# Kernel optimization log

Hardware: AMD Instinct MI355X
Metric: run time of the kernel (lower is better)

## Reference

```python
import jax, jax.numpy as jnp
import numpy as np

B, T, C_EMBD, C_ATT = 16, 1024, 2048, 2048


def wkv(time_decay, time_first, k, v):
    """Numerically-stable RWKV WKV recurrence (matches wkv_cuda).
    time_decay/time_first: [C]; k, v: [B, T, C] -> y: [B, T, C]."""
    w = -jnp.exp(time_decay)  # [C], decay is -exp(param)
    u = time_first
    Bn, Tn, Cn = k.shape

    def step(carry, kv_t):
        aa, bb, pp = carry          # each [B, C]
        kt, vt = kv_t               # [B, C]
        ww = u + kt
        p = jnp.maximum(pp, ww)
        e1 = jnp.exp(pp - p)
        e2 = jnp.exp(ww - p)
        y = (e1 * aa + e2 * vt) / (e1 * bb + e2)
        ww2 = pp + w
        p2 = jnp.maximum(ww2, kt)
        e1b = jnp.exp(ww2 - p2)
        e2b = jnp.exp(kt - p2)
        new = (e1b * aa + e2b * vt, e1b * bb + e2b, p2)
        return new, y

    init = (jnp.zeros((Bn, Cn), k.dtype),
            jnp.zeros((Bn, Cn), k.dtype),
            jnp.full((Bn, Cn), -1e38, k.dtype))
    kT = jnp.swapaxes(k, 0, 1)  # [T, B, C]
    vT = jnp.swapaxes(v, 0, 1)
    _, ys = jax.lax.scan(step, init, (kT, vT))
    return jnp.swapaxes(ys, 0, 1)  # [B, T, C]


def setup_inputs() -> dict:
    key = jax.random.key(0)
    ks = jax.random.split(key, 10)
    xav = np.sqrt(2.0 / (C_EMBD + C_ATT))
    inp = {
        "x": jax.random.normal(ks[0], (B, T, C_EMBD), jnp.float32),
        "time_decay": jax.random.normal(ks[1], (C_ATT,), jnp.float32) * 0.02,
        "time_first": jax.random.normal(ks[2], (C_ATT,), jnp.float32) * 0.02,
        "time_mix_k": jax.random.normal(ks[3], (1, 1, C_EMBD), jnp.float32) * 0.02,
        "time_mix_v": jax.random.normal(ks[4], (1, 1, C_EMBD), jnp.float32) * 0.02,
        "time_mix_r": jax.random.normal(ks[5], (1, 1, C_EMBD), jnp.float32) * 0.02,
        "key_w": jax.random.normal(ks[6], (C_ATT, C_EMBD), jnp.float32) * xav,
        "value_w": jax.random.normal(ks[7], (C_ATT, C_EMBD), jnp.float32) * xav,
        "receptance_w": jax.random.normal(ks[8], (C_ATT, C_EMBD), jnp.float32) * xav,
        "output_w": jax.random.normal(ks[9], (C_EMBD, C_ATT), jnp.float32) * xav,
    }
    return inp


def reference(x, time_decay, time_first, time_mix_k, time_mix_v, time_mix_r,
              key_w, value_w, receptance_w, output_w):
    # time shift: xx[:, t] = x[:, t-1], xx[:, 0] = 0
    xx = jnp.pad(x, ((0, 0), (1, 0), (0, 0)))[:, :-1]
    xk = x * time_mix_k + xx * (1 - time_mix_k)
    xv = x * time_mix_v + xx * (1 - time_mix_v)
    xr = x * time_mix_r + xx * (1 - time_mix_r)
    k = jnp.einsum('btc,dc->btd', xk, key_w)
    v = jnp.einsum('btc,dc->btd', xv, value_w)
    r = jnp.einsum('btc,dc->btd', xr, receptance_w)
    sr = jax.nn.sigmoid(r)
    rwkv = sr * wkv(time_decay, time_first, k, v)
    return jnp.einsum('btd,cd->btc', rwkv, output_w)
```

## Files before the change

### kernel.cpp

```cpp
#include <hip/hip_runtime.h>
#include <hip/hip_bf16.h>

#define BB 16
#define TT 1024
#define CC 2048
#define TS 32

typedef __attribute__((ext_vector_type(4))) float f32x4;
typedef __attribute__((ext_vector_type(8))) short bf16x8;

__device__ __forceinline__ unsigned short f2bf(float f) {
  union { float f; unsigned u; } x; x.f = f;
  unsigned r = x.u + 0x7fffu + ((x.u >> 16) & 1u);
  return (unsigned short)(r >> 16);
}
__device__ __forceinline__ float bf2f(unsigned short u) {
  union { unsigned u; float f; } x; x.u = ((unsigned)u) << 16;
  return x.f;
}

__device__ __forceinline__ ushort4 mix4(float4 a, float4 b, float4 m) {
  ushort4 o;
  o.x = f2bf(a.x * m.x + b.x * (1.f - m.x));
  o.y = f2bf(a.y * m.y + b.y * (1.f - m.y));
  o.z = f2bf(a.z * m.z + b.z * (1.f - m.z));
  o.w = f2bf(a.w * m.w + b.w * (1.f - m.w));
  return o;
}

__global__ void f2bf_all(const float* __restrict__ w0, const float* __restrict__ w1,
                         const float* __restrict__ w2, const float* __restrict__ w3,
                         unsigned short* __restrict__ o0, unsigned short* __restrict__ o1,
                         unsigned short* __restrict__ o2, unsigned short* __restrict__ o3,
                         int n4each) {
  const float* ws[4] = {w0, w1, w2, w3};
  unsigned short* os[4] = {o0, o1, o2, o3};
  int total = 4 * n4each;
  for (int i = blockIdx.x * blockDim.x + threadIdx.x; i < total;
       i += gridDim.x * blockDim.x) {
    int seg = i / n4each, j = i - seg * n4each;
    float4 v = ((const float4*)ws[seg])[j];
    ushort4 o;
    o.x = f2bf(v.x); o.y = f2bf(v.y); o.z = f2bf(v.z); o.w = f2bf(v.w);
    ((ushort4*)os[seg])[j] = o;
  }
}

__global__ void mix_kernel(const float* __restrict__ x,
                           const float* __restrict__ tmk,
                           const float* __restrict__ tmv,
                           const float* __restrict__ tmr,
                           unsigned short* __restrict__ xk,
                           unsigned short* __restrict__ xv,
                           unsigned short* __restrict__ xr,
                           int t0, int Tc) {
  const int C4 = CC / 4;
  const int total = BB * Tc * C4;
  for (int g = blockIdx.x * blockDim.x + threadIdx.x; g < total;
       g += gridDim.x * blockDim.x) {
    int cg = g % C4;
    int lrow = g / C4;
    int tl = lrow % Tc;
    int b = lrow / Tc;
    int t = t0 + tl;
    size_t gidx = (size_t)(b * TT + t) * C4 + cg;
    float4 xc = ((const float4*)x)[gidx];
    float4 xp = make_float4(0.f, 0.f, 0.f, 0.f);
    if (t > 0) xp = ((const float4*)x)[gidx - C4];
    ((ushort4*)xk)[g] = mix4(xc, xp, ((const float4*)tmk)[cg]);
    ((ushort4*)xv)[g] = mix4(xc, xp, ((const float4*)tmv)[cg]);
    ((ushort4*)xr)[g] = mix4(xc, xp, ((const float4*)tmr)[cg]);
  }
}

template<bool BF16OUT>
__global__ __launch_bounds__(512, 2)
void gemm256(const unsigned short* __restrict__ A,
             const unsigned short* __restrict__ B,
             void* __restrict__ Cv, int N, int K, int tcShift, int t0) {
  __shared__ __align__(1024) unsigned char lds[131072];
  const int tid = threadIdx.x;
  const int lane = tid & 63;
  const int wid = tid >> 6;
  const int wr = wid >> 2;
  const int wc = wid & 3;
  const bool grpA = (wid < 4);

  const int nwg = gridDim.x;
  const int cpx = nwg >> 3;
  const int bid = blockIdx.x;
  const int wg = (bid & 7) * cpx + (bid >> 3);
  const int bcolN = N >> 8;
  const int brow = wg / bcolN;
  const int bcol = wg % bcolN;

  const int strow = tid >> 2;
  const int scelem = (((tid & 3) ^ ((tid >> 3) & 3)) << 3);
  const unsigned short* sA0 = A + (size_t)(brow * 256 + strow) * K + scelem;
  const unsigned short* sA1 = A + (size_t)(brow * 256 + 128 + strow) * K + scelem;
  const unsigned short* sB0 = B + (size_t)(bcol * 256 + strow) * K + scelem;
  const unsigned short* sB1 = B + (size_t)(bcol * 256 + 128 + strow) * K + scelem;

  const int frow = lane & 15;
  const int fhi = (lane >> 4) << 4;
  const int fsw = ((frow >> 1) & 3) << 4;
  const int aOff = (wr * 128 + frow) * 64 + (fhi ^ fsw);
  const int bOff = 65536 + (wc * 64 + frow) * 64 + (fhi ^ fsw);
  const int ldsW = wid * 1024;

#define STG(ptr, ldsOff, eoff)                                                 \
  __builtin_amdgcn_global_load_lds(                                            \
      (const __attribute__((address_space(1))) void*)((ptr) + (eoff)),         \
      (__attribute__((address_space(3))) void*)(lds + (ldsOff) + ldsW),        \
      16, 0, 0)
#define STAGE_TILE(BUF, eoff) do {                                             \
    STG(sA0, (BUF) * 16384, eoff);                                             \
    STG(sA1, (BUF) * 16384 + 8192, eoff);                                      \
    STG(sB0, 65536 + (BUF) * 16384, eoff);                                     \
    STG(sB1, 65536 + (BUF) * 16384 + 8192, eoff);                              \
  } while (0)

#define RDT(BUF) do {                                                          \
    _Pragma("unroll") for (int am = 0; am < 8; ++am)                           \
      af[am] = *(const bf16x8*)(lds + aOff + (BUF) * 16384 + am * 1024);       \
    _Pragma("unroll") for (int an = 0; an < 4; ++an)                           \
      bf[an] = *(const bf16x8*)(lds + bOff + (BUF) * 16384 + an * 1024);       \
  } while (0)

#define MFMAT do {                                                             \
    __builtin_amdgcn_s_setprio(1);                                             \
    _Pragma("unroll") for (int am = 0; am < 8; ++am)                           \
    _Pragma("unroll") for (int an = 0; an < 4; ++an)                           \
      acc[am][an] = __builtin_amdgcn_mfma_f32_16x16x32_bf16(                   \
          af[am], bf[an], acc[am][an], 0, 0, 0);                               \
    __builtin_amdgcn_s_setprio(0);                                             \
  } while (0)

#define SB __builtin_amdgcn_sched_barrier(0)
#define BAR __builtin_amdgcn_s_barrier()
#define VMC(n) asm volatile("s_waitcnt vmcnt(" #n ")" ::: "memory")

  f32x4 acc[8][4] = {};
  bf16x8 af[8], bf[4];

  STAGE_TILE(0, 0);
  STAGE_TILE(1, 32);
  SB;
  VMC(4);
  BAR;
  SB;

  for (int g = 0; g < 15; ++g) {
#define TILE_BODY(J)                                                           \
    STAGE_TILE((J + 2) & 3, (2 + J) * 32);                                     \
    if (grpA) RDT(J & 3);                                                      \
    SB;                                                                        \
    VMC(4);                                                                    \
    BAR;                                                                       \
    SB;                                                                        \
    if (!grpA) RDT(J & 3);                                                     \
    MFMAT;
    TILE_BODY(0)
    TILE_BODY(1)
    TILE_BODY(2)
    TILE_BODY(3)
#undef TILE_BODY
    sA0 += 128; sA1 += 128; sB0 += 128; sB1 += 128;
  }

  STAGE_TILE(2, 64);
  if (grpA) RDT(0);
  SB; VMC(4); BAR; SB;
  if (!grpA) RDT(0);
  MFMAT;
  STAGE_TILE(3, 96);
  if (grpA) RDT(1);
  SB; VMC(4); BAR; SB;
  if (!grpA) RDT(1);
  MFMAT;
  if (grpA) RDT(2);
  SB; VMC(0); BAR; SB;
  if (!grpA) RDT(2);
  MFMAT;
  RDT(3);
  MFMAT;

#undef STG
#undef STAGE_TILE
#undef RDT
#undef MFMAT
#undef SB
#undef BAR
#undef VMC

  const int crow0 = (lane >> 4) << 2;
  const int ccol = lane & 15;
  const int tcMask = (1 << tcShift) - 1;
#pragma unroll
  for (int am = 0; am < 8; ++am)
#pragma unroll
    for (int an = 0; an < 4; ++an) {
      const int col = bcol * 256 + wc * 64 + an * 16 + ccol;
#pragma unroll
      for (int j = 0; j < 4; ++j) {
        int r = brow * 256 + wr * 128 + am * 16 + crow0 + j;
        int orow = ((r >> tcShift) << 10) + t0 + (r & tcMask);
        if (BF16OUT)
          ((unsigned short*)Cv)[(size_t)orow * N + col] = f2bf(acc[am][an][j]);
        else
          ((float*)Cv)[(size_t)orow * N + col] = acc[am][an][j];
      }
    }
}

__global__ void wkv_part(const float* __restrict__ time_decay,
                         const unsigned short* __restrict__ k,
                         const unsigned short* __restrict__ v,
                         float* __restrict__ paA, float* __restrict__ paB,
                         float* __restrict__ paP, int Tc) {
  int idx = blockIdx.x * blockDim.x + threadIdx.x;
  int c = idx & (CC - 1);
  int b = (idx >> 11) & (BB - 1);
  int s = idx >> 15;
  float w = -__expf(time_decay[c]);
  float aa = 0.f, bb = 0.f, pp = -1e38f;
  size_t base = ((size_t)b * Tc + s * TS) * CC + c;
  for (int t = 0; t < TS; ++t) {
    size_t off = base + (size_t)t * CC;
    float kt = bf2f(k[off]), vt = bf2f(v[off]);
    float ww2 = pp + w;
    float p2 = fmaxf(ww2, kt);
    float e1 = __expf(ww2 - p2), e2 = __expf(kt - p2);
    aa = e1 * aa + e2 * vt;
    bb = e1 * bb + e2;
    pp = p2;
  }
  paA[idx] = aa; paB[idx] = bb; paP[idx] = pp;
}

__global__ void wkv_comb(const float* __restrict__ time_decay,
                         const float* __restrict__ paA,
                         const float* __restrict__ paB,
                         const float* __restrict__ paP,
                         float* __restrict__ inA, float* __restrict__ inB,
                         float* __restrict__ inP,
                         float* __restrict__ state, int S, int t0) {
  int idx = blockIdx.x * blockDim.x + threadIdx.x;
  int c = idx & (CC - 1);
  float w = -__expf(time_decay[c]);
  float wTs = w * (float)TS;
  float A, Bv, P;
  if (t0 == 0) { A = 0.f; Bv = 0.f; P = -1e38f; }
  else { A = state[idx]; Bv = state[32768 + idx]; P = state[65536 + idx]; }
  for (int s = 0; s < S; ++s) {
    size_t o = (size_t)s * 32768 + idx;
    inA[o] = A; inB[o] = Bv; inP[o] = P;
    float Pd = P + wTs;
    float Ps = paP[o];
    float Pn = fmaxf(Pd, Ps);
    float e1 = __expf(Pd - Pn), e2 = __expf(Ps - Pn);
    A = e1 * A + e2 * paA[o];
    Bv = e1 * Bv + e2 * paB[o];
    P = Pn;
  }
  state[idx] = A; state[32768 + idx] = Bv; state[65536 + idx] = P;
}

__global__ void wkv_out(const float* __restrict__ time_decay,
                        const float* __restrict__ time_first,
                        const unsigned short* __restrict__ k,
                        const unsigned short* __restrict__ v,
                        const unsigned short* __restrict__ r,
                        unsigned short* __restrict__ rwkv,
                        const float* __restrict__ inA,
                        const float* __restrict__ inB,
                        const float* __restrict__ inP, int Tc) {
  int idx = blockIdx.x * blockDim.x + threadIdx.x;
  int c = idx & (CC - 1);
  int b = (idx >> 11) & (BB - 1);
  int s = idx >> 15;
  float w = -__expf(time_decay[c]);
  float u = time_first[c];
  float aa = inA[idx], bb = inB[idx], pp = inP[idx];
  size_t base = ((size_t)b * Tc + s * TS) * CC + c;
  for (int t = 0; t < TS; ++t) {
    size_t off = base + (size_t)t * CC;
    float kt = bf2f(k[off]), vt = bf2f(v[off]);
    float ww = u + kt;
    float p = fmaxf(pp, ww);
    float e1 = __expf(pp - p), e2 = __expf(ww - p);
    float y = (e1 * aa + e2 * vt) / (e1 * bb + e2);
    float rr = bf2f(r[off]);
    float sr = 1.f / (1.f + __expf(-rr));
    rwkv[off] = f2bf(sr * y);
    float ww2 = pp + w;
    float p2 = fmaxf(ww2, kt);
    float e1b = __expf(ww2 - p2), e2b = __expf(kt - p2);
    aa = e1b * aa + e2b * vt;
    bb = e1b * bb + e2b;
    pp = p2;
  }
}

extern "C" void kernel_launch(void* const* d_in, const int* in_sizes, int n_in,
                              void* d_out, int out_size, void* d_ws,
                              size_t ws_size, hipStream_t stream) {
  const float* x          = (const float*)d_in[0];
  const float* time_decay = (const float*)d_in[1];
  const float* time_first = (const float*)d_in[2];
  const float* tmk        = (const float*)d_in[3];
  const float* tmv        = (const float*)d_in[4];
  const float* tmr        = (const float*)d_in[5];
  const float* key_w      = (const float*)d_in[6];
  const float* value_w    = (const float*)d_in[7];
  const float* rec_w      = (const float*)d_in[8];
  const float* out_w      = (const float*)d_in[9];
  float* out = (float*)d_out;

  const size_t WW = (size_t)CC * CC;
  const size_t wtBytes = 4 * WW * 2;
  const size_t stBytes = 3 * (size_t)BB * CC * 4;

  int Tc = 1024;
  while (Tc > 32) {
    size_t chunkBytes = (size_t)BB * Tc * CC * 12;
    if (wtBytes + stBytes + chunkBytes + 1024 <= ws_size) break;
    Tc >>= 1;
  }
  const int Mc = BB * Tc;
  const size_t NC = (size_t)Mc * CC;
  const int S = Tc / TS;

  char* p = (char*)d_ws;
  unsigned short* wk  = (unsigned short*)p; p += WW * 2;
  unsigned short* wv  = (unsigned short*)p; p += WW * 2;
  unsigned short* wrr = (unsigned short*)p; p += WW * 2;
  unsigned short* wo  = (unsigned short*)p; p += WW * 2;
  float* state        = (float*)p;          p += stBytes;
  unsigned short* kbuf= (unsigned short*)p; p += NC * 2;
  unsigned short* vbuf= (unsigned short*)p; p += NC * 2;
  unsigned short* xk  = (unsigned short*)p; p += NC * 2;
  unsigned short* xv  = (unsigned short*)p; p += NC * 2;
  unsigned short* xr  = (unsigned short*)p; p += NC * 2;
  unsigned short* rbuf= (unsigned short*)p; p += NC * 2;
  unsigned short* rwkv = xk;

  const size_t SBt = (size_t)S * 32768;
  float* paA = (float*)xv;
  float* paB = paA + SBt;
  float* paP = paB + SBt;
  float* inA = paP + SBt;
  float* inB = inA + SBt;
  float* inP = inB + SBt;

  f2bf_all<<<2048, 256, 0, stream>>>(key_w, value_w, rec_w, out_w,
                                     wk, wv, wrr, wo, (int)(WW / 4));

  int tcShift = 0;
  while ((1 << tcShift) < Tc) ++tcShift;

  const int nwg = (Mc / 256) * (CC / 256);
  int mixBlocks = (Mc * (CC / 4) + 255) / 256;
  if (mixBlocks > 4096) mixBlocks = 4096;

  for (int t0 = 0; t0 < TT; t0 += Tc) {
    mix_kernel<<<mixBlocks, 256, 0, stream>>>(x, tmk, tmv, tmr, xk, xv, xr,
                                              t0, Tc);
    gemm256<true><<<nwg, 512, 0, stream>>>(xk, wk, kbuf, CC, CC, 10, 0);
    gemm256<true><<<nwg, 512, 0, stream>>>(xv, wv, vbuf, CC, CC, 10, 0);
    wkv_part<<<S * 128, 256, 0, stream>>>(time_decay, kbuf, vbuf,
                                          paA, paB, paP, Tc);
    gemm256<true><<<nwg, 512, 0, stream>>>(xr, wrr, rbuf, CC, CC, 10, 0);
    wkv_comb<<<128, 256, 0, stream>>>(time_decay, paA, paB, paP,
                                      inA, inB, inP, state, S, t0);
    wkv_out<<<S * 128, 256, 0, stream>>>(time_decay, time_first, kbuf, vbuf,
                                         rbuf, rwkv, inA, inB, inP, Tc);
    gemm256<false><<<nwg, 512, 0, stream>>>(rwkv, wo, out, CC, CC,
                                            tcShift, t0);
  }
}
```

Measured before the change: 738.6 us.

## Prefetch next tile's LDS fragments during MFMAs and deepen global staging

```diff
diff --git a/kernel.cpp b/kernel.cpp
--- a/kernel.cpp
+++ b/kernel.cpp
@@ -84,7 +84,6 @@
   const int wid = tid >> 6;
   const int wr = wid >> 2;
   const int wc = wid & 3;
-  const bool grpA = (wid < 4);
 
   const int nwg = gridDim.x;
   const int cpx = nwg >> 3;
@@ -120,19 +119,22 @@
     STG(sB1, 65536 + (BUF) * 16384 + 8192, eoff);                              \
   } while (0)
 
-#define RDT(BUF) do {                                                          \
-    _Pragma("unroll") for (int am = 0; am < 8; ++am)                           \
-      af[am] = *(const bf16x8*)(lds + aOff + (BUF) * 16384 + am * 1024);       \
+#define RD_A_HALF(BUF, BASE) do {                                              \
+    _Pragma("unroll") for (int m = 0; m < 4; ++m)                              \
+      af[(BASE) + m] = *(const bf16x8*)(lds + aOff + (BUF) * 16384 +           \
+                                        ((BASE) + m) * 1024);                  \
+  } while (0)
+#define RD_B(BUF) do {                                                         \
     _Pragma("unroll") for (int an = 0; an < 4; ++an)                           \
       bf[an] = *(const bf16x8*)(lds + bOff + (BUF) * 16384 + an * 1024);       \
   } while (0)
 
-#define MFMAT do {                                                             \
+#define MFMA_HALF(BASE) do {                                                   \
     __builtin_amdgcn_s_setprio(1);                                             \
-    _Pragma("unroll") for (int am = 0; am < 8; ++am)                           \
+    _Pragma("unroll") for (int m = 0; m < 4; ++m)                              \
     _Pragma("unroll") for (int an = 0; an < 4; ++an)                           \
-      acc[am][an] = __builtin_amdgcn_mfma_f32_16x16x32_bf16(                   \
-          af[am], bf[an], acc[am][an], 0, 0, 0);                               \
+      acc[(BASE) + m][an] = __builtin_amdgcn_mfma_f32_16x16x32_bf16(           \
+          af[(BASE) + m], bf[an], acc[(BASE) + m][an], 0, 0, 0);               \
     __builtin_amdgcn_s_setprio(0);                                             \
   } while (0)
 
@@ -145,21 +147,25 @@
 
   STAGE_TILE(0, 0);
   STAGE_TILE(1, 32);
+  STAGE_TILE(2, 64);
   SB;
   VMC(4);
   BAR;
   SB;
+  RD_A_HALF(0, 0); RD_A_HALF(0, 4); RD_B(0);
 
   for (int g = 0; g < 15; ++g) {
 #define TILE_BODY(J)                                                           \
-    STAGE_TILE((J + 2) & 3, (2 + J) * 32);                                     \
-    if (grpA) RDT(J & 3);                                                      \
+    STAGE_TILE((J + 3) & 3, (3 + J) * 32);                                     \
+    MFMA_HALF(0);                                                              \
+    RD_A_HALF((J + 1) & 3, 0);                                                 \
+    MFMA_HALF(4);                                                              \
+    RD_A_HALF((J + 1) & 3, 4);                                                 \
     SB;                                                                        \
     VMC(4);                                                                    \
     BAR;                                                                       \
     SB;                                                                        \
-    if (!grpA) RDT(J & 3);                                                     \
-    MFMAT;
+    RD_B((J + 1) & 3);
     TILE_BODY(0)
     TILE_BODY(1)
     TILE_BODY(2)
@@ -168,27 +174,32 @@
     sA0 += 128; sA1 += 128; sB0 += 128; sB1 += 128;
   }
 
-  STAGE_TILE(2, 64);
-  if (grpA) RDT(0);
+  STAGE_TILE(3, 96);
+  MFMA_HALF(0);
+  RD_A_HALF(1, 0);
+  MFMA_HALF(4);
+  RD_A_HALF(1, 4);
   SB; VMC(4); BAR; SB;
-  if (!grpA) RDT(0);
-  MFMAT;
-  STAGE_TILE(3, 96);
-  if (grpA) RDT(1);
-  SB; VMC(4); BAR; SB;
-  if (!grpA) RDT(1);
-  MFMAT;
-  if (grpA) RDT(2);
+  RD_B(1);
+  MFMA_HALF(0);
+  RD_A_HALF(2, 0);
+  MFMA_HALF(4);
+  RD_A_HALF(2, 4);
   SB; VMC(0); BAR; SB;
-  if (!grpA) RDT(2);
-  MFMAT;
-  RDT(3);
-  MFMAT;
+  RD_B(2);
+  MFMA_HALF(0);
+  RD_A_HALF(3, 0);
+  MFMA_HALF(4);
+  RD_A_HALF(3, 4);
+  RD_B(3);
+  MFMA_HALF(0);
+  MFMA_HALF(4);
 
 #undef STG
 #undef STAGE_TILE
-#undef RDT
-#undef MFMAT
+#undef RD_A_HALF
+#undef RD_B
+#undef MFMA_HALF
 #undef SB
 #undef BAR
 #undef VMC
```

Measured after the change: 725.4 us. Within noise of the previous version (-1.8%).
